# Kernel optimization log

Measured on AMD Instinct MI355X. Metric: run time of the kernel, lower is better.

Reference implementation:

```python
import jax, jax.numpy as jnp
import numpy as np

N_NODES = 100000
N_EDGES = 1600000
IN_DIM = 128
HID_DIM = 128


def gcn_conv(x, W, b, src, dst, n_nodes):
    # PyG GCNConv: linear (no bias) -> symmetric degree norm with self-loops -> scatter-add -> +bias
    h = x @ W  # [N, H]
    e = src.shape[0]
    deg = jax.ops.segment_sum(jnp.ones((e,), dtype=h.dtype), dst, num_segments=n_nodes) + 1.0  # +1 self-loop
    dinv = deg ** -0.5  # deg >= 1 always
    norm = dinv[src] * dinv[dst]  # [E]
    agg = jax.ops.segment_sum(h[src] * norm[:, None], dst, num_segments=n_nodes)
    agg = agg + h * (dinv * dinv)[:, None]  # self-loop contribution
    return agg + b


def setup_inputs() -> dict:
    key = jax.random.key(0)
    ks = jax.random.split(key, 8)
    x = jax.random.normal(ks[0], (N_NODES, IN_DIM), dtype=jnp.float32)
    edge_index = jax.random.randint(ks[1], (2, N_EDGES), 0, N_NODES, dtype=jnp.int32)
    def glorot(k, fan_in, fan_out):
        lim = np.sqrt(6.0 / (fan_in + fan_out)).astype(np.float32)
        return jax.random.uniform(k, (fan_in, fan_out), dtype=jnp.float32, minval=-lim, maxval=lim)
    W1 = glorot(ks[2], IN_DIM, HID_DIM)
    W2 = glorot(ks[3], HID_DIM, HID_DIM)
    W3 = glorot(ks[4], HID_DIM, HID_DIM)
    b1 = jnp.zeros((HID_DIM,), jnp.float32)
    b2 = jnp.zeros((HID_DIM,), jnp.float32)
    b3 = jnp.zeros((HID_DIM,), jnp.float32)
    return {"x": x, "W1": W1, "b1": b1, "W2": W2, "b2": b2, "W3": W3, "b3": b3,
            "edge_index": edge_index}


def reference(x, W1, b1, W2, b2, W3, b3, edge_index):
    src, dst = edge_index[0], edge_index[1]
    n = x.shape[0]
    z = jax.nn.relu(gcn_conv(x, W1, b1, src, dst, n))
    z = jax.nn.relu(gcn_conv(z, W2, b2, src, dst, n))
    z = gcn_conv(z, W3, b3, src, dst, n)
    # edge dot-product decode on the same edge set
    logits = jnp.sum(z[src] * z[dst], axis=1)  # [E]
    return jax.nn.sigmoid(logits)
```

## Files before the change

kernel.cpp:

```cpp
#include <hip/hip_runtime.h>
#include <math.h>

#define NN 100000
#define NE 1600000
#define DIM 128
#define SCHUNK 1024
#define NBK 391
#define ECH 4096

typedef unsigned short u16;
typedef unsigned int u32;
typedef __attribute__((ext_vector_type(8))) short bf16x8;
typedef __attribute__((ext_vector_type(4))) float f32x4;

__device__ inline u16 f2bf(float f) {
  union { float f; u32 u; } v; v.f = f;
  u32 r = v.u + 0x7FFF + ((v.u >> 16) & 1);
  return (u16)(r >> 16);
}
__device__ inline float bflo(u32 u) { union { u32 u; float f; } v; v.u = u << 16; return v.f; }
__device__ inline float bfhi(u32 u) { union { u32 u; float f; } v; v.u = u & 0xFFFF0000u; return v.f; }
__device__ inline float sigm(float x) { return 1.0f / (1.0f + expf(-x)); }

__global__ void k_deg(const int* __restrict__ dst, int* __restrict__ deg) {
  int i = blockIdx.x * blockDim.x + threadIdx.x;
  if (i < NE) atomicAdd(&deg[dst[i]], 1);
}

__global__ void k_scan1(const int* __restrict__ deg, int* __restrict__ bsum) {
  __shared__ int sd[256];
  int t = threadIdx.x;
  int base = blockIdx.x * SCHUNK + t * 4;
  int s = 0;
#pragma unroll
  for (int j = 0; j < 4; ++j) { int idx = base + j; if (idx < NN) s += deg[idx]; }
  sd[t] = s; __syncthreads();
  for (int off = 128; off > 0; off >>= 1) {
    if (t < off) sd[t] += sd[t + off];
    __syncthreads();
  }
  if (t == 0) bsum[blockIdx.x] = sd[0];
}

__global__ void k_scan2(int* __restrict__ bsum, int nb) {
  __shared__ int sd[128];
  int t = threadIdx.x;
  int v = (t < nb) ? bsum[t] : 0;
  sd[t] = v; __syncthreads();
  for (int off = 1; off < 128; off <<= 1) {
    int x = (t >= off) ? sd[t - off] : 0;
    __syncthreads();
    sd[t] += x;
    __syncthreads();
  }
  if (t < nb) bsum[t] = sd[t] - v;
}

__global__ void k_scan3(const int* __restrict__ deg, const int* __restrict__ bsum,
                        int* __restrict__ offs, float* __restrict__ dinv) {
  __shared__ int ts[256];
  int t = threadIdx.x;
  int base = blockIdx.x * SCHUNK + t * 4;
  int v[4]; int loc = 0;
#pragma unroll
  for (int j = 0; j < 4; ++j) { int idx = base + j; v[j] = (idx < NN) ? deg[idx] : 0; loc += v[j]; }
  ts[t] = loc; __syncthreads();
  for (int off = 1; off < 256; off <<= 1) {
    int x = (t >= off) ? ts[t - off] : 0;
    __syncthreads();
    ts[t] += x;
    __syncthreads();
  }
  int run = bsum[blockIdx.x] + ts[t] - loc;
#pragma unroll
  for (int j = 0; j < 4; ++j) {
    int idx = base + j;
    if (idx < NN) {
      offs[idx] = run;
      dinv[idx] = rsqrtf((float)v[j] + 1.0f);
    }
    run += v[j];
  }
}

__launch_bounds__(256)
__global__ void k_bucket(const int* __restrict__ src, const int* __restrict__ dst,
                         const int* __restrict__ offs, int* __restrict__ bcur,
                         uint2* __restrict__ bstage) {
  __shared__ int cnt[512];
  __shared__ int bl[512];
  __shared__ int gb[512];
  __shared__ int tmp[256];
  __shared__ uint2 st[ECH];
  int t = threadIdx.x;
  int e0 = blockIdx.x * ECH;
  cnt[t] = 0; cnt[t + 256] = 0;
  __syncthreads();
  int b_[16], r_[16]; u32 s_[16], y_[16];
#pragma unroll
  for (int k = 0; k < 16; ++k) {
    int i = e0 + k * 256 + t;
    b_[k] = -1;
    if (i < NE) {
      int d = dst[i];
      int bb = d >> 8;
      b_[k] = bb;
      s_[k] = (u32)src[i];
      y_[k] = ((u32)(d & 255) << 21) | (u32)i;
      r_[k] = atomicAdd(&cnt[bb], 1);
    }
  }
  __syncthreads();
  int c0 = cnt[2 * t], c1 = cnt[2 * t + 1];
  tmp[t] = c0 + c1;
  __syncthreads();
  for (int off = 1; off < 256; off <<= 1) {
    int v = (t >= off) ? tmp[t - off] : 0;
    __syncthreads();
    tmp[t] += v;
    __syncthreads();
  }
  int excl = tmp[t] - (c0 + c1);
  bl[2 * t] = excl; bl[2 * t + 1] = excl + c0;
  __syncthreads();
#pragma unroll
  for (int k = 0; k < 16; ++k)
    if (b_[k] >= 0) st[bl[b_[k]] + r_[k]] = make_uint2(s_[k], y_[k]);
  for (int b = t; b < 512; b += 256) {
    int n = cnt[b];
    gb[b] = (n > 0) ? atomicAdd(&bcur[b], n) : 0;
  }
  __syncthreads();
  for (int b = t; b < 512; b += 256) {
    int n = cnt[b];
    if (n > 0) {
      uint2* dp = bstage + offs[b << 8] + gb[b];
      const uint2* sp = st + bl[b];
      for (int j = 0; j < n; ++j) dp[j] = sp[j];
    }
  }
}

__launch_bounds__(256)
__global__ void k_fillb(const uint2* __restrict__ bstage, const int* __restrict__ offs,
                        int* __restrict__ csr_src, int* __restrict__ csr_dst,
                        int* __restrict__ csr_eid) {
  __shared__ int curl[256];
  int t = threadIdx.x;
  int b = blockIdx.x;
  int nb0 = b << 8;
  curl[t] = 0;
  __syncthreads();
  int sbase = offs[nb0];
  int send = (b == NBK - 1) ? NE : offs[nb0 + 256];
  for (int j = sbase + t; j < send; j += 256) {
    uint2 e = bstage[j];
    int dl = e.y >> 21;
    int eid = e.y & 0x1FFFFF;
    int pos = offs[nb0 + dl] + atomicAdd(&curl[dl], 1);
    csr_src[pos] = (int)e.x;
    csr_dst[pos] = nb0 + dl;
    csr_eid[pos] = eid;
  }
}

__global__ void k_pack3(const float* __restrict__ W1, const float* __restrict__ W2,
                        const float* __restrict__ W3, u16* __restrict__ Wp1,
                        u16* __restrict__ Wp2, u16* __restrict__ Wp3) {
  int gid = blockIdx.x * blockDim.x + threadIdx.x;
  int which = gid >> 14;
  int tid = gid & 16383;
  const float* W = which == 0 ? W1 : (which == 1 ? W2 : W3);
  u16* Wp = which == 0 ? Wp1 : (which == 1 ? Wp2 : Wp3);
  int b = tid & 7, j = (tid >> 3) & 15, kb = (tid >> 7) & 3, ks = (tid >> 9) & 3, ct = tid >> 11;
  int k = ks * 32 + kb * 8 + b, col = ct * 16 + j;
  Wp[tid] = f2bf(W[k * 128 + col]);
}

__launch_bounds__(256)
__global__ void k_gemm1(const float* __restrict__ X, const u16* __restrict__ Wp,
                        const float* __restrict__ dinv, u16* __restrict__ hp) {
  __shared__ u16 wl[16384];
  __shared__ u16 ctile[4][2048];
  int t = threadIdx.x;
  int w = t >> 6, l = t & 63;
  int row0 = blockIdx.x * 64;
  int rbase = row0 + w * 16;

#pragma unroll
  for (int i = 0; i < 8; ++i) {
    int off = (i * 256 + t) * 8;
    *(uint4*)&wl[off] = *(const uint4*)&Wp[off];
  }
  __syncthreads();

  int arow = rbase + (l & 15);
  arow = arow < NN ? arow : NN - 1;
  const float* ab = X + (size_t)arow * DIM + (l >> 4) * 8;
  bf16x8 a[4];
#pragma unroll
  for (int ks = 0; ks < 4; ++ks) {
    float4 f0 = *(const float4*)(ab + ks * 32);
    float4 f1 = *(const float4*)(ab + ks * 32 + 4);
    bf16x8 aa;
    aa[0] = (short)f2bf(f0.x); aa[1] = (short)f2bf(f0.y);
    aa[2] = (short)f2bf(f0.z); aa[3] = (short)f2bf(f0.w);
    aa[4] = (short)f2bf(f1.x); aa[5] = (short)f2bf(f1.y);
    aa[6] = (short)f2bf(f1.z); aa[7] = (short)f2bf(f1.w);
    a[ks] = aa;
  }

  f32x4 acc[8];
#pragma unroll
  for (int ct = 0; ct < 8; ++ct) {
    acc[ct] = (f32x4){0.f, 0.f, 0.f, 0.f};
#pragma unroll
    for (int ks = 0; ks < 4; ++ks) {
      bf16x8 bfr = *(const bf16x8*)&wl[ct * 2048 + ks * 512 + (l >> 4) * 128 + (l & 15) * 8];
      acc[ct] = __builtin_amdgcn_mfma_f32_16x16x32_bf16(a[ks], bfr, acc[ct], 0, 0, 0);
    }
  }

  float dv[4];
#pragma unroll
  for (int v = 0; v < 4; ++v) {
    int rr = rbase + (l >> 4) * 4 + v;
    dv[v] = dinv[rr < NN ? rr : NN - 1];
  }
  u16* ct_lds = ctile[w];
#pragma unroll
  for (int ct = 0; ct < 8; ++ct) {
#pragma unroll
    for (int v = 0; v < 4; ++v) {
      int row = (l >> 4) * 4 + v;
      ct_lds[row * DIM + ct * 16 + (l & 15)] = f2bf(dv[v] * acc[ct][v]);
    }
  }
  __syncthreads();
#pragma unroll
  for (int rr = 0; rr < 4; ++rr) {
    int row = rr * 4 + (l >> 4);
    int grow = rbase + row;
    if (grow < NN)
      *(uint4*)&hp[(size_t)grow * DIM + (l & 15) * 8] =
          *(const uint4*)&ct_lds[row * DIM + (l & 15) * 8];
  }
}

__launch_bounds__(256)
__global__ void k_fused(const u16* __restrict__ hp, const int* __restrict__ csr_src,
                        const int* __restrict__ offs, const int* __restrict__ deg,
                        const float* __restrict__ dinv, const float* __restrict__ bias,
                        const u16* __restrict__ Wp, u16* __restrict__ hpo) {
  __shared__ u16 atile[8192];
  int t = threadIdx.x;
  int row0 = blockIdx.x * 64;

  {
    int g = t >> 5, l = t & 31;
    const uint2* hp2 = (const uint2*)hp;
    float4 bb = ((const float4*)bias)[l];
    for (int pass = 0; pass < 8; ++pass) {
      int row = pass * 8 + g;
      int n = row0 + row;
      int nn = n < NN ? n : NN - 1;
      float dn = dinv[nn];
      int s = offs[nn], cnt = deg[nn];
      float a0 = 0.f, a1 = 0.f, a2 = 0.f, a3 = 0.f;
      int i = 0;
      for (; i + 8 <= cnt; i += 8) {
        int u[8];
#pragma unroll
        for (int k = 0; k < 8; ++k) u[k] = csr_src[s + i + k];
        uint2 v[8];
#pragma unroll
        for (int k = 0; k < 8; ++k) v[k] = hp2[(size_t)u[k] * 32 + l];
#pragma unroll
        for (int k = 0; k < 8; ++k) {
          a0 += bflo(v[k].x); a1 += bfhi(v[k].x); a2 += bflo(v[k].y); a3 += bfhi(v[k].y);
        }
      }
      for (; i + 4 <= cnt; i += 4) {
        int u[4];
#pragma unroll
        for (int k = 0; k < 4; ++k) u[k] = csr_src[s + i + k];
        uint2 v[4];
#pragma unroll
        for (int k = 0; k < 4; ++k) v[k] = hp2[(size_t)u[k] * 32 + l];
#pragma unroll
        for (int k = 0; k < 4; ++k) {
          a0 += bflo(v[k].x); a1 += bfhi(v[k].x); a2 += bflo(v[k].y); a3 += bfhi(v[k].y);
        }
      }
      for (; i < cnt; ++i) {
        int u = csr_src[s + i];
        uint2 v = hp2[(size_t)u * 32 + l];
        a0 += bflo(v.x); a1 += bfhi(v.x); a2 += bflo(v.y); a3 += bfhi(v.y);
      }
      uint2 sv = hp2[(size_t)nn * 32 + l];
      float r0 = fmaxf(dn * (a0 + bflo(sv.x)) + bb.x, 0.f);
      float r1 = fmaxf(dn * (a1 + bfhi(sv.x)) + bb.y, 0.f);
      float r2 = fmaxf(dn * (a2 + bflo(sv.y)) + bb.z, 0.f);
      float r3 = fmaxf(dn * (a3 + bfhi(sv.y)) + bb.w, 0.f);
      ushort4 o; o.x = f2bf(r0); o.y = f2bf(r1); o.z = f2bf(r2); o.w = f2bf(r3);
      int byte = row * 256 + ((l * 8) ^ ((row & 7) << 4));
      *(ushort4*)((char*)atile + byte) = o;
    }
  }
  __syncthreads();

  int w = t >> 6, l = t & 63;
  int rbase = row0 + w * 16;
  int arow = w * 16 + (l & 15);
  bf16x8 a[4];
#pragma unroll
  for (int ks = 0; ks < 4; ++ks) {
    int cb = ((l >> 4) * 16 + ks * 64) ^ ((arow & 7) << 4);
    a[ks] = *(const bf16x8*)((const char*)atile + arow * 256 + cb);
  }
  f32x4 acc[8];
#pragma unroll
  for (int ct = 0; ct < 8; ++ct) {
    acc[ct] = (f32x4){0.f, 0.f, 0.f, 0.f};
#pragma unroll
    for (int ks = 0; ks < 4; ++ks) {
      bf16x8 bfr = *(const bf16x8*)&Wp[ct * 2048 + ks * 512 + (l >> 4) * 128 + (l & 15) * 8];
      acc[ct] = __builtin_amdgcn_mfma_f32_16x16x32_bf16(a[ks], bfr, acc[ct], 0, 0, 0);
    }
  }
  __syncthreads();

  float dv[4];
#pragma unroll
  for (int v = 0; v < 4; ++v) {
    int rr = rbase + (l >> 4) * 4 + v;
    dv[v] = dinv[rr < NN ? rr : NN - 1];
  }
  u16* ct_lds = atile + w * 2048;
#pragma unroll
  for (int ct = 0; ct < 8; ++ct) {
#pragma unroll
    for (int v = 0; v < 4; ++v) {
      int row = (l >> 4) * 4 + v;
      ct_lds[row * DIM + ct * 16 + (l & 15)] = f2bf(dv[v] * acc[ct][v]);
    }
  }
  __syncthreads();
#pragma unroll
  for (int rr = 0; rr < 4; ++rr) {
    int row = rr * 4 + (l >> 4);
    int grow = rbase + row;
    if (grow < NN)
      *(uint4*)&hpo[(size_t)grow * DIM + (l & 15) * 8] =
          *(const uint4*)&ct_lds[row * DIM + (l & 15) * 8];
  }
}

__launch_bounds__(256)
__global__ void k_agg(const u16* __restrict__ hp, const int* __restrict__ csr_src,
                      const int* __restrict__ offs, const int* __restrict__ deg,
                      const float* __restrict__ dinv, const float* __restrict__ bias,
                      u16* __restrict__ outb) {
  int t = threadIdx.x;
  int g = t >> 5, l = t & 31;
  int n = blockIdx.x * 8 + g;
  float dn = dinv[n];
  int s = offs[n], cnt = deg[n];
  const uint2* hp2 = (const uint2*)hp;
  float a0 = 0.f, a1 = 0.f, a2 = 0.f, a3 = 0.f;
  int i = 0;
  for (; i + 8 <= cnt; i += 8) {
    int u[8];
#pragma unroll
    for (int k = 0; k < 8; ++k) u[k] = csr_src[s + i + k];
    uint2 v[8];
#pragma unroll
    for (int k = 0; k < 8; ++k) v[k] = hp2[(size_t)u[k] * 32 + l];
#pragma unroll
    for (int k = 0; k < 8; ++k) {
      a0 += bflo(v[k].x); a1 += bfhi(v[k].x); a2 += bflo(v[k].y); a3 += bfhi(v[k].y);
    }
  }
  for (; i + 4 <= cnt; i += 4) {
    int u[4];
#pragma unroll
    for (int k = 0; k < 4; ++k) u[k] = csr_src[s + i + k];
    uint2 v[4];
#pragma unroll
    for (int k = 0; k < 4; ++k) v[k] = hp2[(size_t)u[k] * 32 + l];
#pragma unroll
    for (int k = 0; k < 4; ++k) {
      a0 += bflo(v[k].x); a1 += bfhi(v[k].x); a2 += bflo(v[k].y); a3 += bfhi(v[k].y);
    }
  }
  for (; i < cnt; ++i) {
    int u = csr_src[s + i];
    uint2 v = hp2[(size_t)u * 32 + l];
    a0 += bflo(v.x); a1 += bfhi(v.x); a2 += bflo(v.y); a3 += bfhi(v.y);
  }
  uint2 sv = hp2[(size_t)n * 32 + l];
  float4 bb = ((const float4*)bias)[l];
  float r0 = dn * (a0 + bflo(sv.x)) + bb.x;
  float r1 = dn * (a1 + bfhi(sv.x)) + bb.y;
  float r2 = dn * (a2 + bflo(sv.y)) + bb.z;
  float r3 = dn * (a3 + bfhi(sv.y)) + bb.w;
  ushort4 o; o.x = f2bf(r0); o.y = f2bf(r1); o.z = f2bf(r2); o.w = f2bf(r3);
  *(ushort4*)&outb[(size_t)n * DIM + l * 4] = o;
}

__launch_bounds__(256)
__global__ void k_decode_mfma(const u16* __restrict__ z, const int* __restrict__ csr_src,
                              const int* __restrict__ csr_dst, const int* __restrict__ csr_eid,
                              float* __restrict__ out) {
  int l = threadIdx.x & 63;
  int wid = blockIdx.x * 4 + (threadIdx.x >> 6);
  int r = l & 15, g = l >> 4;
  int tile0 = wid * 8;
  for (int tt = 0; tt < 8; ++tt) {
    int p0 = (tile0 + tt) * 16;
    int s = csr_src[p0 + r];
    int d = csr_dst[p0 + r];
    int e = csr_eid[p0 + r];
    const bf16x8* za = (const bf16x8*)(z + (size_t)s * DIM + g * 8);
    const bf16x8* zb = (const bf16x8*)(z + (size_t)d * DIM + g * 8);
    f32x4 acc = (f32x4){0.f, 0.f, 0.f, 0.f};
#pragma unroll
    for (int ks = 0; ks < 4; ++ks)
      acc = __builtin_amdgcn_mfma_f32_16x16x32_bf16(za[ks * 4], zb[ks * 4], acc, 0, 0, 0);
    if ((r >> 2) == g) out[e] = sigm(acc[r & 3]);
  }
}

extern "C" void kernel_launch(void* const* d_in, const int* in_sizes, int n_in,
                              void* d_out, int out_size, void* d_ws, size_t ws_size,
                              hipStream_t stream) {
  const float* x  = (const float*)d_in[0];
  const float* W1 = (const float*)d_in[1];
  const float* b1 = (const float*)d_in[2];
  const float* W2 = (const float*)d_in[3];
  const float* b2 = (const float*)d_in[4];
  const float* W3 = (const float*)d_in[5];
  const float* b3 = (const float*)d_in[6];
  const int*   ei = (const int*)d_in[7];
  const int* src = ei;
  const int* dst = ei + NE;
  float* out = (float*)d_out;

  char* w = (char*)d_ws;
  size_t p = 0;
  auto alloc = [&](size_t bytes) -> void* {
    void* r = w + p;
    p += (bytes + 255) & ~(size_t)255;
    return r;
  };
  int*   deg     = (int*)alloc((size_t)NN * 4);
  int*   offs    = (int*)alloc((size_t)NN * 4);
  float* dinv    = (float*)alloc((size_t)NN * 4);
  int*   bsum    = (int*)alloc(1024);
  int*   bcur    = (int*)alloc(512 * 4);
  uint2* bstage  = (uint2*)alloc((size_t)NE * 8);
  int*   csr_src = (int*)alloc((size_t)NE * 4);
  int*   csr_dst = (int*)alloc((size_t)NE * 4);
  int*   csr_eid = (int*)alloc((size_t)NE * 4);
  u16*   hp      = (u16*)alloc((size_t)NN * DIM * 2);
  u16*   hb      = (u16*)alloc((size_t)NN * DIM * 2);
  u16*   zb      = (u16*)alloc((size_t)NN * DIM * 2);
  u16*   Wp1     = (u16*)alloc(16384 * 2);
  u16*   Wp2     = (u16*)alloc(16384 * 2);
  u16*   Wp3     = (u16*)alloc(16384 * 2);
  (void)in_sizes; (void)n_in; (void)out_size; (void)ws_size;

  hipMemsetAsync(deg, 0, (size_t)NN * 4, stream);
  hipMemsetAsync(bcur, 0, 512 * 4, stream);

  k_deg<<<(NE + 255) / 256, 256, 0, stream>>>(dst, deg);
  int nb = (NN + SCHUNK - 1) / SCHUNK;
  k_scan1<<<nb, 256, 0, stream>>>(deg, bsum);
  k_scan2<<<1, 128, 0, stream>>>(bsum, nb);
  k_scan3<<<nb, 256, 0, stream>>>(deg, bsum, offs, dinv);

  int cb = (NE + ECH - 1) / ECH;
  k_bucket<<<cb, 256, 0, stream>>>(src, dst, offs, bcur, bstage);
  k_fillb<<<NBK, 256, 0, stream>>>(bstage, offs, csr_src, csr_dst, csr_eid);

  k_pack3<<<192, 256, 0, stream>>>(W1, W2, W3, Wp1, Wp2, Wp3);

  int gb = (NN + 63) / 64;
  k_gemm1<<<gb, 256, 0, stream>>>(x, Wp1, dinv, hp);
  k_fused<<<gb, 256, 0, stream>>>(hp, csr_src, offs, deg, dinv, b1, Wp2, hb);
  k_fused<<<gb, 256, 0, stream>>>(hb, csr_src, offs, deg, dinv, b2, Wp3, hp);
  k_agg <<<NN / 8, 256, 0, stream>>>(hp, csr_src, offs, deg, dinv, b3, zb);
  k_decode_mfma<<<3125, 256, 0, stream>>>(zb, csr_src, csr_dst, csr_eid, out);
}
```

Before: 478.4 us.

## Halve fused-layer tile to 32 rows, split GEMM columns across waves, pad LDS

The fused aggregate+GEMM kernel now handles 32 nodes per block instead of 64. The four waves split the output into two row groups and two column halves, which doubles the grid and cuts LDS use so more blocks fit per CU for the latency-bound gather. k_gemm1 stops staging W in LDS, reads the packed weights straight from global/L2, and pads its output tile rows to 136 to avoid bank conflicts. The risk is more redundant weight loads from global memory. The bounds checks were dropped, which relies on NN being divisible by 32.

```diff
diff --git a/kernel.cpp b/kernel.cpp
--- a/kernel.cpp
+++ b/kernel.cpp
@@ -180,19 +180,11 @@
 __launch_bounds__(256)
 __global__ void k_gemm1(const float* __restrict__ X, const u16* __restrict__ Wp,
                         const float* __restrict__ dinv, u16* __restrict__ hp) {
-  __shared__ u16 wl[16384];
-  __shared__ u16 ctile[4][2048];
+  __shared__ u16 ctile[4][2176];
   int t = threadIdx.x;
   int w = t >> 6, l = t & 63;
   int row0 = blockIdx.x * 64;
   int rbase = row0 + w * 16;
-
-#pragma unroll
-  for (int i = 0; i < 8; ++i) {
-    int off = (i * 256 + t) * 8;
-    *(uint4*)&wl[off] = *(const uint4*)&Wp[off];
-  }
-  __syncthreads();
 
   int arow = rbase + (l & 15);
   arow = arow < NN ? arow : NN - 1;
@@ -216,7 +208,7 @@
     acc[ct] = (f32x4){0.f, 0.f, 0.f, 0.f};
 #pragma unroll
     for (int ks = 0; ks < 4; ++ks) {
-      bf16x8 bfr = *(const bf16x8*)&wl[ct * 2048 + ks * 512 + (l >> 4) * 128 + (l & 15) * 8];
+      bf16x8 bfr = *(const bf16x8*)&Wp[ct * 2048 + ks * 512 + (l >> 4) * 128 + (l & 15) * 8];
       acc[ct] = __builtin_amdgcn_mfma_f32_16x16x32_bf16(a[ks], bfr, acc[ct], 0, 0, 0);
     }
   }
@@ -233,7 +225,7 @@
 #pragma unroll
     for (int v = 0; v < 4; ++v) {
       int row = (l >> 4) * 4 + v;
-      ct_lds[row * DIM + ct * 16 + (l & 15)] = f2bf(dv[v] * acc[ct][v]);
+      ct_lds[row * 136 + ct * 16 + (l & 15)] = f2bf(dv[v] * acc[ct][v]);
     }
   }
   __syncthreads();
@@ -243,7 +235,7 @@
     int grow = rbase + row;
     if (grow < NN)
       *(uint4*)&hp[(size_t)grow * DIM + (l & 15) * 8] =
-          *(const uint4*)&ct_lds[row * DIM + (l & 15) * 8];
+          *(const uint4*)&ct_lds[row * 136 + (l & 15) * 8];
   }
 }
 
@@ -252,20 +244,19 @@
                         const int* __restrict__ offs, const int* __restrict__ deg,
                         const float* __restrict__ dinv, const float* __restrict__ bias,
                         const u16* __restrict__ Wp, u16* __restrict__ hpo) {
-  __shared__ u16 atile[8192];
-  int t = threadIdx.x;
-  int row0 = blockIdx.x * 64;
+  __shared__ u16 atile[4352];
+  int t = threadIdx.x;
+  int row0 = blockIdx.x * 32;
 
   {
     int g = t >> 5, l = t & 31;
     const uint2* hp2 = (const uint2*)hp;
     float4 bb = ((const float4*)bias)[l];
-    for (int pass = 0; pass < 8; ++pass) {
+    for (int pass = 0; pass < 4; ++pass) {
       int row = pass * 8 + g;
       int n = row0 + row;
-      int nn = n < NN ? n : NN - 1;
-      float dn = dinv[nn];
-      int s = offs[nn], cnt = deg[nn];
+      float dn = dinv[n];
+      int s = offs[n], cnt = deg[n];
       float a0 = 0.f, a1 = 0.f, a2 = 0.f, a3 = 0.f;
       int i = 0;
       for (; i + 8 <= cnt; i += 8) {
@@ -297,7 +288,7 @@
         uint2 v = hp2[(size_t)u * 32 + l];
         a0 += bflo(v.x); a1 += bfhi(v.x); a2 += bflo(v.y); a3 += bfhi(v.y);
       }
-      uint2 sv = hp2[(size_t)nn * 32 + l];
+      uint2 sv = hp2[(size_t)n * 32 + l];
       float r0 = fmaxf(dn * (a0 + bflo(sv.x)) + bb.x, 0.f);
       float r1 = fmaxf(dn * (a1 + bfhi(sv.x)) + bb.y, 0.f);
       float r2 = fmaxf(dn * (a2 + bflo(sv.y)) + bb.z, 0.f);
@@ -310,21 +301,23 @@
   __syncthreads();
 
   int w = t >> 6, l = t & 63;
-  int rbase = row0 + w * 16;
-  int arow = w * 16 + (l & 15);
+  int rbase = row0 + (w & 1) * 16;
+  int arow = (w & 1) * 16 + (l & 15);
+  int chalf = w >> 1;
   bf16x8 a[4];
 #pragma unroll
   for (int ks = 0; ks < 4; ++ks) {
     int cb = ((l >> 4) * 16 + ks * 64) ^ ((arow & 7) << 4);
     a[ks] = *(const bf16x8*)((const char*)atile + arow * 256 + cb);
   }
-  f32x4 acc[8];
-#pragma unroll
-  for (int ct = 0; ct < 8; ++ct) {
+  f32x4 acc[4];
+#pragma unroll
+  for (int ct = 0; ct < 4; ++ct) {
+    int ctg = chalf * 4 + ct;
     acc[ct] = (f32x4){0.f, 0.f, 0.f, 0.f};
 #pragma unroll
     for (int ks = 0; ks < 4; ++ks) {
-      bf16x8 bfr = *(const bf16x8*)&Wp[ct * 2048 + ks * 512 + (l >> 4) * 128 + (l & 15) * 8];
+      bf16x8 bfr = *(const bf16x8*)&Wp[ctg * 2048 + ks * 512 + (l >> 4) * 128 + (l & 15) * 8];
       acc[ct] = __builtin_amdgcn_mfma_f32_16x16x32_bf16(a[ks], bfr, acc[ct], 0, 0, 0);
     }
   }
@@ -332,27 +325,23 @@
 
   float dv[4];
 #pragma unroll
-  for (int v = 0; v < 4; ++v) {
-    int rr = rbase + (l >> 4) * 4 + v;
-    dv[v] = dinv[rr < NN ? rr : NN - 1];
-  }
-  u16* ct_lds = atile + w * 2048;
-#pragma unroll
-  for (int ct = 0; ct < 8; ++ct) {
+  for (int v = 0; v < 4; ++v) dv[v] = dinv[rbase + (l >> 4) * 4 + v];
+  u16* ct_lds = atile + w * 1088;
+#pragma unroll
+  for (int ct = 0; ct < 4; ++ct) {
 #pragma unroll
     for (int v = 0; v < 4; ++v) {
       int row = (l >> 4) * 4 + v;
-      ct_lds[row * DIM + ct * 16 + (l & 15)] = f2bf(dv[v] * acc[ct][v]);
-    }
-  }
-  __syncthreads();
-#pragma unroll
-  for (int rr = 0; rr < 4; ++rr) {
-    int row = rr * 4 + (l >> 4);
+      ct_lds[row * 68 + ct * 16 + (l & 15)] = f2bf(dv[v] * acc[ct][v]);
+    }
+  }
+  __syncthreads();
+#pragma unroll
+  for (int rr = 0; rr < 2; ++rr) {
+    int row = rr * 8 + (l >> 3);
     int grow = rbase + row;
-    if (grow < NN)
-      *(uint4*)&hpo[(size_t)grow * DIM + (l & 15) * 8] =
-          *(const uint4*)&ct_lds[row * DIM + (l & 15) * 8];
+    *(uint4*)&hpo[(size_t)grow * DIM + chalf * 64 + (l & 7) * 8] =
+        *(const uint4*)&ct_lds[row * 68 + (l & 7) * 8];
   }
 }
 
@@ -487,8 +476,8 @@
 
   int gb = (NN + 63) / 64;
   k_gemm1<<<gb, 256, 0, stream>>>(x, Wp1, dinv, hp);
-  k_fused<<<gb, 256, 0, stream>>>(hp, csr_src, offs, deg, dinv, b1, Wp2, hb);
-  k_fused<<<gb, 256, 0, stream>>>(hb, csr_src, offs, deg, dinv, b2, Wp3, hp);
+  k_fused<<<NN / 32, 256, 0, stream>>>(hp, csr_src, offs, deg, dinv, b1, Wp2, hb);
+  k_fused<<<NN / 32, 256, 0, stream>>>(hb, csr_src, offs, deg, dinv, b2, Wp3, hp);
   k_agg <<<NN / 8, 256, 0, stream>>>(hp, csr_src, offs, deg, dinv, b3, zb);
   k_decode_mfma<<<3125, 256, 0, stream>>>(zb, csr_src, csr_dst, csr_eid, out);
 }
```

New measurement: 440.2 us. 1.09x faster.
